# Kernel optimization log

Hardware: AMD Instinct MI355X
Metric: run time of the kernel (lower is better)

## Reference

```python
import jax, jax.numpy as jnp
import numpy as np

N_NODES = 100000
N_EDGES = 1600000
HIDDEN = 128
STEPS = 4
N_GRAPHS = 64


def setup_inputs() -> dict:
    key = jax.random.key(0)
    ks = jax.random.split(key, 8)
    x = jax.random.normal(ks[0], (N_NODES, HIDDEN), dtype=jnp.float32)
    edge_index = jax.random.randint(ks[1], (2, N_EDGES), 0, N_NODES, dtype=jnp.int64)
    batch = jnp.sort(jax.random.randint(ks[2], (N_NODES,), 0, N_GRAPHS, dtype=jnp.int64))
    s = 1.0 / np.sqrt(HIDDEN)
    weight = jax.random.normal(ks[3], (STEPS, HIDDEN, HIDDEN), dtype=jnp.float32) * s
    w_ih = jax.random.normal(ks[4], (3 * HIDDEN, HIDDEN), dtype=jnp.float32) * s
    w_hh = jax.random.normal(ks[5], (3 * HIDDEN, HIDDEN), dtype=jnp.float32) * s
    b_ih = jnp.zeros((3 * HIDDEN,), dtype=jnp.float32)
    b_hh = jnp.zeros((3 * HIDDEN,), dtype=jnp.float32)
    return {"x": x, "edge_index": edge_index, "batch": batch,
            "weight": weight, "w_ih": w_ih, "w_hh": w_hh,
            "b_ih": b_ih, "b_hh": b_hh}


def _gru_cell(m, h, w_ih, w_hh, b_ih, b_hh):
    # PyTorch GRUCell: gates ordered (r, z, n)
    gi = m @ w_ih.T + b_ih  # [N, 3H]
    gh = h @ w_hh.T + b_hh  # [N, 3H]
    i_r, i_z, i_n = jnp.split(gi, 3, axis=-1)
    h_r, h_z, h_n = jnp.split(gh, 3, axis=-1)
    r = jax.nn.sigmoid(i_r + h_r)
    z = jax.nn.sigmoid(i_z + h_z)
    n = jnp.tanh(i_n + r * h_n)
    return (1.0 - z) * n + z * h


def reference(x, edge_index, batch, weight, w_ih, w_hh, b_ih, b_hh):
    src, dst = edge_index[0], edge_index[1]
    h = x
    for i in range(STEPS):
        m = h @ weight[i]  # [N, H]
        # message = m[src] scattered (add) into dst
        aggr = jax.ops.segment_sum(m[src], dst, num_segments=N_NODES)
        h = _gru_cell(aggr, h, w_ih, w_hh, b_ih, b_hh)
    h = jax.nn.relu(h)
    # global mean pool per graph
    sums = jax.ops.segment_sum(h, batch, num_segments=N_GRAPHS)  # [G, H]
    counts = jax.ops.segment_sum(jnp.ones((N_NODES,), h.dtype), batch, num_segments=N_GRAPHS)
    return sums / jnp.maximum(counts, 1.0)[:, None]
```

## Files before the change

kernel.cpp:

```cpp
#include <hip/hip_runtime.h>

#define N_NODES  100000
#define N_EDGES  1600000
#define HIDDEN   128
#define STEPS    4
#define N_GRAPHS 64
#define NBUCK    256
#define BWID     391
#define OUT_P    136

typedef unsigned short u16;
typedef unsigned int   u32;
typedef unsigned long long u64;
typedef __attribute__((ext_vector_type(8))) short bf16x8;
typedef __attribute__((ext_vector_type(4))) float f32x4;

__device__ inline u16 f2bf(float f) {
  u32 u = __float_as_uint(f);
  u = (u + 0x7FFFu + ((u >> 16) & 1u)) >> 16;
  return (u16)u;
}
__device__ inline float bf2f(u16 b) { return __uint_as_float(((u32)b) << 16); }

__device__ inline float fast_sig(float x) { return 1.f / (1.f + __expf(-x)); }
__device__ inline float fast_tanh(float x) {
  x = fminf(fmaxf(x, -15.f), 15.f);
  float e = __expf(2.f * x);
  return (e - 1.f) / (e + 1.f);
}

__global__ __launch_bounds__(1024) void k_bhist(const int* __restrict__ edst,
                                                int* __restrict__ bcnt) {
  __shared__ int hist[NBUCK];
  int tid = threadIdx.x;
  if (tid < NBUCK) hist[tid] = 0;
  __syncthreads();
  int e0 = blockIdx.x * 4096;
  #pragma unroll
  for (int i = 0; i < 4; ++i) {
    int e = e0 + i * 1024 + tid;
    if (e < N_EDGES) atomicAdd(&hist[(u32)edst[e] / (u32)BWID], 1);
  }
  __syncthreads();
  if (tid < NBUCK) atomicAdd(&bcnt[tid], hist[tid]);
}

__global__ void k_bscan(const int* __restrict__ bcnt, int* __restrict__ ebase,
                        int* __restrict__ gcursor) {
  __shared__ int buf[NBUCK];
  int t = threadIdx.x;
  int v = bcnt[t];
  buf[t] = v;
  __syncthreads();
  for (int off = 1; off < NBUCK; off <<= 1) {
    int u = 0;
    if (t >= off) u = buf[t - off];
    __syncthreads();
    buf[t] += u;
    __syncthreads();
  }
  int ex = buf[t] - v;
  ebase[t] = ex;
  gcursor[t] = ex;
  if (t == NBUCK - 1) ebase[NBUCK] = buf[t];
}

__global__ __launch_bounds__(1024) void k_part(const int* __restrict__ esrc,
                                               const int* __restrict__ edst,
                                               int* __restrict__ gcursor,
                                               u64* __restrict__ ebuf) {
  __shared__ int hist[NBUCK];
  __shared__ int base[NBUCK];
  int tid = threadIdx.x;
  if (tid < NBUCK) hist[tid] = 0;
  __syncthreads();
  int e0 = blockIdx.x * 4096;
  int sv[4], dv[4], bk[4], rk[4];
  #pragma unroll
  for (int i = 0; i < 4; ++i) {
    int e = e0 + i * 1024 + tid;
    if (e < N_EDGES) {
      sv[i] = esrc[e];
      dv[i] = edst[e];
      bk[i] = (int)((u32)dv[i] / (u32)BWID);
      rk[i] = atomicAdd(&hist[bk[i]], 1);
    } else bk[i] = -1;
  }
  __syncthreads();
  if (tid < NBUCK) base[tid] = atomicAdd(&gcursor[tid], hist[tid]);
  __syncthreads();
  #pragma unroll
  for (int i = 0; i < 4; ++i) {
    if (bk[i] >= 0) {
      int pos = base[bk[i]] + rk[i];
      ebuf[pos] = ((u64)(u32)dv[i] << 32) | (u32)sv[i];
    }
  }
}

__global__ __launch_bounds__(1024) void k_csr(const u64* __restrict__ ebuf,
                                              const int* __restrict__ ebase,
                                              int* __restrict__ offs,
                                              int* __restrict__ csr) {
  __shared__ int lcnt[512];
  __shared__ int lofs[512];
  int b = blockIdx.x, tid = threadIdx.x;
  int n0 = b * BWID;
  int n1 = min(n0 + BWID, N_NODES);
  int nn = n1 - n0;
  int e0 = ebase[b], e1 = ebase[b + 1];
  if (tid < 512) lcnt[tid] = 0;
  __syncthreads();
  for (int e = e0 + tid; e < e1; e += 1024) {
    int dst = (int)(ebuf[e] >> 32);
    atomicAdd(&lcnt[dst - n0], 1);
  }
  __syncthreads();
  if (tid < 512) lofs[tid] = lcnt[tid];
  __syncthreads();
  for (int off = 1; off < 512; off <<= 1) {
    int v = 0;
    if (tid < 512 && tid >= off) v = lofs[tid - off];
    __syncthreads();
    if (tid < 512 && tid >= off) lofs[tid] += v;
    __syncthreads();
  }
  int nodeoff = 0;
  if (tid < 512) nodeoff = e0 + lofs[tid] - lcnt[tid];
  if (tid < 512) lofs[tid] = nodeoff;
  if (tid < nn) offs[n0 + tid] = nodeoff;
  if (b == 0 && tid == 0) offs[N_NODES] = N_EDGES;
  __syncthreads();
  for (int e = e0 + tid; e < e1; e += 1024) {
    u64 p = ebuf[e];
    int src = (int)(p & 0xffffffffull);
    int dst = (int)(p >> 32);
    int pos = atomicAdd(&lofs[dst - n0], 1);
    csr[pos] = src;
  }
}

__global__ void k_wb(const float* __restrict__ W, const float* __restrict__ w_ih,
                     const float* __restrict__ w_hh, u16* __restrict__ bsw) {
  __shared__ float wrow[128];
  int b = blockIdx.x, st = b >> 8, k = b & 255, t = threadIdx.x;
  if (k < 128) wrow[t] = W[(st * 128 + k) * 128 + t];
  __syncthreads();
  int kc = k >> 5, quad = (k >> 3) & 3, kl = k & 7;
  u16* base = bsw + (size_t)st * 131072 + kc * 16384;
  #pragma unroll
  for (int gq = 0; gq < 4; ++gq) {
    int c = gq * 128 + t;
    float v;
    if (k < 128) {
      if (c < 384) {
        const float* wr = w_ih + c * 128;
        float sacc = 0.f;
        for (int j = 0; j < 128; ++j) sacc += wrow[j] * wr[j];
        v = sacc;
      } else v = 0.f;
    } else {
      int kk = k - 128;
      if (c < 256)      v = w_hh[c * 128 + kk];
      else if (c < 384) v = 0.f;
      else              v = w_hh[(c - 128) * 128 + kk];
    }
    int gi = c >> 7, cw = c & 127;
    int wv = cw >> 5, hu = (cw >> 4) & 1, nl = c & 15;
    int slot = wv * 8 + gi * 2 + hu;
    base[(slot * 4 + quad) * 128 + nl * 8 + kl] = f2bf(v);
  }
}

__global__ void k_convert(const float* __restrict__ x, u16* __restrict__ h) {
  int i = (blockIdx.x * 256 + threadIdx.x) * 4;
  float4 v = *(const float4*)(x + i);
  u16 o[4] = {f2bf(v.x), f2bf(v.y), f2bf(v.z), f2bf(v.w)};
  *(uint2*)(h + i) = *(uint2*)o;
}

__device__ inline void acc8(float* a, uint4 p) {
  a[0] += bf2f((u16)(p.x & 0xffffu)); a[1] += bf2f((u16)(p.x >> 16));
  a[2] += bf2f((u16)(p.y & 0xffffu)); a[3] += bf2f((u16)(p.y >> 16));
  a[4] += bf2f((u16)(p.z & 0xffffu)); a[5] += bf2f((u16)(p.z >> 16));
  a[6] += bf2f((u16)(p.w & 0xffffu)); a[7] += bf2f((u16)(p.w >> 16));
}

__global__ void k_gather(const u16* __restrict__ h, const int* __restrict__ csr,
                         const int* __restrict__ offs, u16* __restrict__ s) {
  int node = blockIdx.x * 4 + (threadIdx.x >> 6);
  int lane = threadIdx.x & 63;
  int q   = lane >> 4;
  int sub = lane & 15;
  int beg = offs[node], end = offs[node + 1];
  float a[8] = {0.f, 0.f, 0.f, 0.f, 0.f, 0.f, 0.f, 0.f};
  int j = beg + q;
  for (; j + 12 < end; j += 16) {
    int s0 = csr[j], s1 = csr[j + 4], s2 = csr[j + 8], s3 = csr[j + 12];
    uint4 p0 = *(const uint4*)(h + (size_t)s0 * 128 + sub * 8);
    uint4 p1 = *(const uint4*)(h + (size_t)s1 * 128 + sub * 8);
    uint4 p2 = *(const uint4*)(h + (size_t)s2 * 128 + sub * 8);
    uint4 p3 = *(const uint4*)(h + (size_t)s3 * 128 + sub * 8);
    acc8(a, p0); acc8(a, p1); acc8(a, p2); acc8(a, p3);
  }
  for (; j < end; j += 4) {
    int s0 = csr[j];
    uint4 p0 = *(const uint4*)(h + (size_t)s0 * 128 + sub * 8);
    acc8(a, p0);
  }
  #pragma unroll
  for (int i = 0; i < 8; ++i) {
    a[i] += __shfl_xor(a[i], 16);
    a[i] += __shfl_xor(a[i], 32);
  }
  if (q == 0) {
    uint4 o;
    o.x = (u32)f2bf(a[0]) | ((u32)f2bf(a[1]) << 16);
    o.y = (u32)f2bf(a[2]) | ((u32)f2bf(a[3]) << 16);
    o.z = (u32)f2bf(a[4]) | ((u32)f2bf(a[5]) << 16);
    o.w = (u32)f2bf(a[6]) | ((u32)f2bf(a[7]) << 16);
    *(uint4*)(s + (size_t)node * 128 + sub * 8) = o;
  }
}

__global__ __launch_bounds__(256, 3) void k_gemm_gru(
    const u16* __restrict__ s_mat, const u16* __restrict__ h_mat,
    const u16* __restrict__ bsw, const float* __restrict__ b_ih,
    const float* __restrict__ b_hh, u16* __restrict__ h_out) {
  __shared__ u16 Asw[8192];
  __shared__ u16 Osw[32 * OUT_P];

  const int tid  = threadIdx.x;
  const int wave = tid >> 6;
  const int lane = tid & 63;
  const int nl   = lane & 15;
  const int quad = lane >> 4;
  const int row0 = blockIdx.x * 32;

  {
    int snl = tid & 15, squad = (tid >> 4) & 3, sel = tid >> 6;
    int g = sel & 1, half = sel >> 1;
    const u16* row = (half ? h_mat : s_mat) + (size_t)(row0 + g * 16 + snl) * 128;
    #pragma unroll
    for (int kc2 = 0; kc2 < 4; ++kc2) {
      uint4 v = *(const uint4*)(row + kc2 * 32 + squad * 8);
      *(uint4*)&Asw[(((g * 8 + half * 4 + kc2) * 4 + squad) * 16 + snl) * 8] = v;
    }
  }
  __syncthreads();

  const u16* bp = bsw + wave * 8 * 512 + lane * 8;

  f32x4 acc[2][8];
  #pragma unroll
  for (int g = 0; g < 2; ++g)
    #pragma unroll
    for (int u = 0; u < 8; ++u) acc[g][u] = (f32x4){0.f, 0.f, 0.f, 0.f};

  bf16x8 bcur[6], bnext[6];
  #pragma unroll
  for (int i = 0; i < 6; ++i) bcur[i] = *(const bf16x8*)(bp + i * 512);

  #pragma unroll
  for (int kc = 0; kc < 8; ++kc) {
    if (kc < 7) {
      #pragma unroll
      for (int i = 0; i < 6; ++i) {
        int us = (kc + 1 < 4) ? i : (i < 4 ? i : i + 2);
        bnext[i] = *(const bf16x8*)(bp + (kc + 1) * 16384 + us * 512);
      }
    }
    bf16x8 a0 = *(const bf16x8*)&Asw[kc * 512 + lane * 8];
    bf16x8 a1 = *(const bf16x8*)&Asw[(8 + kc) * 512 + lane * 8];
    #pragma unroll
    for (int i = 0; i < 6; ++i) {
      int u = (kc < 4) ? i : (i < 4 ? i : i + 2);
      acc[0][u] = __builtin_amdgcn_mfma_f32_16x16x32_bf16(a0, bcur[i], acc[0][u], 0, 0, 0);
      acc[1][u] = __builtin_amdgcn_mfma_f32_16x16x32_bf16(a1, bcur[i], acc[1][u], 0, 0, 0);
    }
    #pragma unroll
    for (int i = 0; i < 6; ++i) bcur[i] = bnext[i];
  }

  float bias[8];
  #pragma unroll
  for (int u = 0; u < 8; ++u) {
    int gi = u >> 1, hu = u & 1;
    int cw = wave * 32 + hu * 16 + nl;
    bias[u] = (gi == 0) ? b_ih[cw] + b_hh[cw]
            : (gi == 1) ? b_ih[128 + cw] + b_hh[128 + cw]
            : (gi == 2) ? b_ih[256 + cw]
                        : b_hh[256 + cw];
  }

  #pragma unroll
  for (int g = 0; g < 2; ++g) {
    #pragma unroll
    for (int hu = 0; hu < 2; ++hu) {
      int cw = wave * 32 + hu * 16 + nl;
      int hbase = ((g * 8 + 4 + wave) * 4 + ((hu * 2 + (nl >> 3)) & 3)) * 128 + (nl & 7);
      #pragma unroll
      for (int i = 0; i < 4; ++i) {
        int m = quad * 4 + i;
        float rv = fast_sig(acc[g][0 + hu][i] + bias[0 + hu]);
        float zv = fast_sig(acc[g][2 + hu][i] + bias[2 + hu]);
        float iv = acc[g][4 + hu][i] + bias[4 + hu];
        float hn = acc[g][6 + hu][i] + bias[6 + hu];
        float hv = bf2f(Asw[hbase + m * 8]);
        float n  = fast_tanh(iv + rv * hn);
        float o  = (1.f - zv) * n + zv * hv;
        Osw[(g * 16 + m) * OUT_P + cw] = f2bf(o);
      }
    }
  }
  __syncthreads();

  {
    int r32 = tid >> 3, c0 = (tid & 7) * 16;
    uint4 v0 = *(const uint4*)&Osw[r32 * OUT_P + c0];
    uint4 v1 = *(const uint4*)&Osw[r32 * OUT_P + c0 + 8];
    uint4* dstp = (uint4*)(h_out + (size_t)(row0 + r32) * 128 + c0);
    dstp[0] = v0;
    dstp[1] = v1;
  }
}

__global__ void k_pool_partial(const u16* __restrict__ h, const int* __restrict__ batch,
                               float* __restrict__ acc) {
  int t = threadIdx.x;
  int node0 = blockIdx.x * 125;
  int node1 = node0 + 125;
  int cur = batch[node0];
  float sum = 0.f;
  for (int r = node0; r < node1; ++r) {
    int g = batch[r];
    if (g != cur) {
      atomicAdd(&acc[cur * 128 + t], sum);
      sum = 0.f;
      cur = g;
    }
    sum += fmaxf(bf2f(h[(size_t)r * 128 + t]), 0.f);
  }
  atomicAdd(&acc[cur * 128 + t], sum);
}

__global__ void k_pool_div(const float* __restrict__ acc, const int* __restrict__ batch,
                           float* __restrict__ out) {
  __shared__ int se[2];
  int g = blockIdx.x, t = threadIdx.x;
  if (t < 2) {
    int target = g + t;
    int lo = 0, hi = N_NODES;
    while (lo < hi) { int mid = (lo + hi) >> 1; if (batch[mid] < target) lo = mid + 1; else hi = mid; }
    se[t] = lo;
  }
  __syncthreads();
  int cnt = se[1] - se[0];
  out[g * 128 + t] = acc[g * 128 + t] / (float)(cnt > 0 ? cnt : 1);
}

extern "C" void kernel_launch(void* const* d_in, const int* in_sizes, int n_in,
                              void* d_out, int out_size, void* d_ws, size_t ws_size,
                              hipStream_t stream) {
  const float* x     = (const float*)d_in[0];
  const int*   edges = (const int*)d_in[1];
  const int*   batch = (const int*)d_in[2];
  const float* W     = (const float*)d_in[3];
  const float* w_ih  = (const float*)d_in[4];
  const float* w_hh  = (const float*)d_in[5];
  const float* b_ih  = (const float*)d_in[6];
  const float* b_hh  = (const float*)d_in[7];
  float* out = (float*)d_out;

  char* w = (char*)d_ws;
  u16* buf0    = (u16*)(w);
  u16* buf1    = (u16*)(w + 25600000);
  u16* bsw     = (u16*)(w + 51200000);
  float* acc   = (float*)(w + 52300032);
  int* offs    = (int*)(w + 52710400);
  int* gcursor = (int*)(w + 53120768);
  int* bcnt    = (int*)(w + 53122048);
  int* ebase   = (int*)(w + 53123328);
  int* csr     = (int*)(w + 53531136);
  u64* ebuf    = (u64*)buf1;

  const int* esrc = edges;
  const int* edst = edges + N_EDGES;

  hipMemsetAsync(bcnt, 0, NBUCK * sizeof(int), stream);
  k_bhist<<<391, 1024, 0, stream>>>(edst, bcnt);
  k_bscan<<<1, NBUCK, 0, stream>>>(bcnt, ebase, gcursor);
  k_part<<<391, 1024, 0, stream>>>(esrc, edst, gcursor, ebuf);
  k_csr<<<NBUCK, 1024, 0, stream>>>(ebuf, ebase, offs, csr);
  k_wb<<<1024, 128, 0, stream>>>(W, w_ih, w_hh, bsw);
  k_convert<<<(N_NODES * HIDDEN) / 1024, 256, 0, stream>>>(x, buf0);
  hipMemsetAsync(acc, 0, N_GRAPHS * HIDDEN * sizeof(float), stream);

  u16* hcur = buf0;
  u16* hnxt = buf1;
  for (int st = 0; st < STEPS; ++st) {
    k_gather<<<N_NODES / 4, 256, 0, stream>>>(hcur, csr, offs, hnxt);
    k_gemm_gru<<<N_NODES / 32, 256, 0, stream>>>(hnxt, hcur, bsw + st * 131072,
                                                 b_ih, b_hh, hnxt);
    u16* tmp = hcur; hcur = hnxt; hnxt = tmp;
  }
  k_pool_partial<<<800, 128, 0, stream>>>(hcur, batch, acc);
  k_pool_div<<<N_GRAPHS, 128, 0, stream>>>(acc, batch, out);
}
```

Measured before the change: 642.9 us.

## Drop histogram pass via fixed-capacity buckets, write GRU output directly

The edge partition now writes into fixed-capacity per-bucket slots (BCAP), so the separate histogram kernel and its pre-scan disappear; the scan runs after partitioning to produce CSR offsets. The GEMM-GRU epilogue removes the LDS staging buffer and its sync, storing bf16 results straight to global memory, and uses hardware reciprocal for sigmoid/tanh. This saves a full pass over the edge destinations and a kernel launch, but relies on no bucket exceeding 7168 edges (the mean is about 6250), and the direct 2-byte scattered stores are less coalesced than the previous 16-byte row writes.

```diff
diff --git a/kernel.cpp b/kernel.cpp
--- a/kernel.cpp
+++ b/kernel.cpp
@@ -7,7 +7,7 @@
 #define N_GRAPHS 64
 #define NBUCK    256
 #define BWID     391
-#define OUT_P    136
+#define BCAP     7168
 
 typedef unsigned short u16;
 typedef unsigned int   u32;
@@ -22,48 +22,9 @@
 }
 __device__ inline float bf2f(u16 b) { return __uint_as_float(((u32)b) << 16); }
 
-__device__ inline float fast_sig(float x) { return 1.f / (1.f + __expf(-x)); }
-__device__ inline float fast_tanh(float x) {
-  x = fminf(fmaxf(x, -15.f), 15.f);
-  float e = __expf(2.f * x);
-  return (e - 1.f) / (e + 1.f);
-}
-
-__global__ __launch_bounds__(1024) void k_bhist(const int* __restrict__ edst,
-                                                int* __restrict__ bcnt) {
-  __shared__ int hist[NBUCK];
-  int tid = threadIdx.x;
-  if (tid < NBUCK) hist[tid] = 0;
-  __syncthreads();
-  int e0 = blockIdx.x * 4096;
-  #pragma unroll
-  for (int i = 0; i < 4; ++i) {
-    int e = e0 + i * 1024 + tid;
-    if (e < N_EDGES) atomicAdd(&hist[(u32)edst[e] / (u32)BWID], 1);
-  }
-  __syncthreads();
-  if (tid < NBUCK) atomicAdd(&bcnt[tid], hist[tid]);
-}
-
-__global__ void k_bscan(const int* __restrict__ bcnt, int* __restrict__ ebase,
-                        int* __restrict__ gcursor) {
-  __shared__ int buf[NBUCK];
-  int t = threadIdx.x;
-  int v = bcnt[t];
-  buf[t] = v;
-  __syncthreads();
-  for (int off = 1; off < NBUCK; off <<= 1) {
-    int u = 0;
-    if (t >= off) u = buf[t - off];
-    __syncthreads();
-    buf[t] += u;
-    __syncthreads();
-  }
-  int ex = buf[t] - v;
-  ebase[t] = ex;
-  gcursor[t] = ex;
-  if (t == NBUCK - 1) ebase[NBUCK] = buf[t];
-}
+__device__ inline float rcp_f(float x) { return __builtin_amdgcn_rcpf(x); }
+__device__ inline float sig_f(float x) { return rcp_f(1.f + __expf(-x)); }
+__device__ inline float tanh_f(float x) { return 1.f - 2.f * rcp_f(1.f + __expf(2.f * x)); }
 
 __global__ __launch_bounds__(1024) void k_part(const int* __restrict__ esrc,
                                                const int* __restrict__ edst,
@@ -92,10 +53,27 @@
   #pragma unroll
   for (int i = 0; i < 4; ++i) {
     if (bk[i] >= 0) {
-      int pos = base[bk[i]] + rk[i];
+      int pos = bk[i] * BCAP + base[bk[i]] + rk[i];
       ebuf[pos] = ((u64)(u32)dv[i] << 32) | (u32)sv[i];
     }
   }
+}
+
+__global__ void k_bscan(const int* __restrict__ gcursor, int* __restrict__ ebase) {
+  __shared__ int buf[NBUCK];
+  int t = threadIdx.x;
+  int v = gcursor[t];
+  buf[t] = v;
+  __syncthreads();
+  for (int off = 1; off < NBUCK; off <<= 1) {
+    int u = 0;
+    if (t >= off) u = buf[t - off];
+    __syncthreads();
+    buf[t] += u;
+    __syncthreads();
+  }
+  ebase[t] = buf[t] - v;
+  if (t == NBUCK - 1) ebase[NBUCK] = buf[t];
 }
 
 __global__ __launch_bounds__(1024) void k_csr(const u64* __restrict__ ebuf,
@@ -108,11 +86,13 @@
   int n0 = b * BWID;
   int n1 = min(n0 + BWID, N_NODES);
   int nn = n1 - n0;
-  int e0 = ebase[b], e1 = ebase[b + 1];
+  int e0 = ebase[b];
+  int cnt = ebase[b + 1] - e0;
+  const u64* ebase_p = ebuf + (size_t)b * BCAP;
   if (tid < 512) lcnt[tid] = 0;
   __syncthreads();
-  for (int e = e0 + tid; e < e1; e += 1024) {
-    int dst = (int)(ebuf[e] >> 32);
+  for (int e = tid; e < cnt; e += 1024) {
+    int dst = (int)(ebase_p[e] >> 32);
     atomicAdd(&lcnt[dst - n0], 1);
   }
   __syncthreads();
@@ -131,8 +111,8 @@
   if (tid < nn) offs[n0 + tid] = nodeoff;
   if (b == 0 && tid == 0) offs[N_NODES] = N_EDGES;
   __syncthreads();
-  for (int e = e0 + tid; e < e1; e += 1024) {
-    u64 p = ebuf[e];
+  for (int e = tid; e < cnt; e += 1024) {
+    u64 p = ebase_p[e];
     int src = (int)(p & 0xffffffffull);
     int dst = (int)(p >> 32);
     int pos = atomicAdd(&lofs[dst - n0], 1);
@@ -228,7 +208,6 @@
     const u16* __restrict__ bsw, const float* __restrict__ b_ih,
     const float* __restrict__ b_hh, u16* __restrict__ h_out) {
   __shared__ u16 Asw[8192];
-  __shared__ u16 Osw[32 * OUT_P];
 
   const int tid  = threadIdx.x;
   const int wave = tid >> 6;
@@ -302,26 +281,16 @@
       #pragma unroll
       for (int i = 0; i < 4; ++i) {
         int m = quad * 4 + i;
-        float rv = fast_sig(acc[g][0 + hu][i] + bias[0 + hu]);
-        float zv = fast_sig(acc[g][2 + hu][i] + bias[2 + hu]);
+        float rv = sig_f(acc[g][0 + hu][i] + bias[0 + hu]);
+        float zv = sig_f(acc[g][2 + hu][i] + bias[2 + hu]);
         float iv = acc[g][4 + hu][i] + bias[4 + hu];
         float hn = acc[g][6 + hu][i] + bias[6 + hu];
         float hv = bf2f(Asw[hbase + m * 8]);
-        float n  = fast_tanh(iv + rv * hn);
-        float o  = (1.f - zv) * n + zv * hv;
-        Osw[(g * 16 + m) * OUT_P + cw] = f2bf(o);
+        float n  = tanh_f(iv + rv * hn);
+        float o  = n + zv * (hv - n);
+        h_out[(size_t)(row0 + g * 16 + m) * 128 + cw] = f2bf(o);
       }
     }
-  }
-  __syncthreads();
-
-  {
-    int r32 = tid >> 3, c0 = (tid & 7) * 16;
-    uint4 v0 = *(const uint4*)&Osw[r32 * OUT_P + c0];
-    uint4 v1 = *(const uint4*)&Osw[r32 * OUT_P + c0 + 8];
-    uint4* dstp = (uint4*)(h_out + (size_t)(row0 + r32) * 128 + c0);
-    dstp[0] = v0;
-    dstp[1] = v1;
   }
 }
 
@@ -379,7 +348,6 @@
   float* acc   = (float*)(w + 52300032);
   int* offs    = (int*)(w + 52710400);
   int* gcursor = (int*)(w + 53120768);
-  int* bcnt    = (int*)(w + 53122048);
   int* ebase   = (int*)(w + 53123328);
   int* csr     = (int*)(w + 53531136);
   u64* ebuf    = (u64*)buf1;
@@ -387,10 +355,9 @@
   const int* esrc = edges;
   const int* edst = edges + N_EDGES;
 
-  hipMemsetAsync(bcnt, 0, NBUCK * sizeof(int), stream);
-  k_bhist<<<391, 1024, 0, stream>>>(edst, bcnt);
-  k_bscan<<<1, NBUCK, 0, stream>>>(bcnt, ebase, gcursor);
+  hipMemsetAsync(gcursor, 0, NBUCK * sizeof(int), stream);
   k_part<<<391, 1024, 0, stream>>>(esrc, edst, gcursor, ebuf);
+  k_bscan<<<1, NBUCK, 0, stream>>>(gcursor, ebase);
   k_csr<<<NBUCK, 1024, 0, stream>>>(ebuf, ebase, offs, csr);
   k_wb<<<1024, 128, 0, stream>>>(W, w_ih, w_hh, bsw);
   k_convert<<<(N_NODES * HIDDEN) / 1024, 256, 0, stream>>>(x, buf0);
```

Result: faster. 598.0 us (-7.0%).
